# Performance work log

Measured on AMD Instinct MI355X. Metric: run time of the kernel, lower is better.

Reference implementation:

```python
import jax, jax.numpy as jnp
import numpy as np
import math

B, L, D = 2, 2048, 768
H, DK = 8, 64
DV = D // H  # 96
N_POS = 32
DFF = 2 * D
EPS = 1e-5


def setup_inputs() -> dict:
    key = jax.random.key(0)
    ks = jax.random.split(key, 12)
    s = 0.02
    return {
        "x": jax.random.normal(ks[0], (B, L, D), jnp.float32),
        "norm1_w": jnp.ones((D,), jnp.float32),
        "norm2_w": jnp.ones((D,), jnp.float32),
        "wq": jax.random.normal(ks[1], (D, H * DK), jnp.float32) * s,
        "wk": jax.random.normal(ks[2], (D, H * DK), jnp.float32) * s,
        "wv": jax.random.normal(ks[3], (D, H * DV), jnp.float32) * s,
        "wo": jax.random.normal(ks[4], (H * DV, D), jnp.float32) * s,
        "bo": jnp.zeros((D,), jnp.float32),
        "u_param": jax.random.normal(ks[5], (H, DK), jnp.float32) * s,
        "v_param": jax.random.normal(ks[6], (H, DK), jnp.float32) * s,
        "w_pos": jax.random.normal(ks[7], (H, DK, N_POS), jnp.float32) * s,
        "w1": jax.random.normal(ks[8], (D, DFF), jnp.float32) * s,
        "b1": jnp.zeros((DFF,), jnp.float32),
        "w2": jax.random.normal(ks[9], (DFF, D), jnp.float32) * s,
        "b2": jnp.zeros((D,), jnp.float32),
    }


def _rel_basis(l: int, n: int) -> jnp.ndarray:
    # Enformer-style central-mask relative position basis: [l, l, n]
    pos = jnp.arange(l)
    distance = pos[None, :] - pos[:, None]  # [l, l]
    pow_rate = jnp.exp(jnp.log(jnp.float32((l + 1) / 2.0)) / (n // 2))
    center_widths = pow_rate ** jnp.arange(1, n // 2 + 1, dtype=jnp.float32)
    d = distance[:, :, None].astype(jnp.float32)
    unsigned = (jnp.abs(d) <= center_widths).astype(jnp.float32)
    signed = jnp.sign(d) * unsigned
    return jnp.concatenate([unsigned, signed], axis=-1)  # [l, l, n]


def _rmsnorm(x, w):
    norm = jnp.mean(x * x, axis=-1, keepdims=True)
    return x * jax.lax.rsqrt(norm + EPS) * w


def reference(x, norm1_w, norm2_w, wq, wk, wv, wo, bo,
              u_param, v_param, w_pos, w1, b1, w2, b2):
    b, l, _ = x.shape
    skip = x
    h1 = _rmsnorm(x, norm1_w)

    q = (h1 @ wq).reshape(b, l, H, DK)
    k = (h1 @ wk).reshape(b, l, H, DK)
    v = (h1 @ wv).reshape(b, l, H, DV)

    basis = _rel_basis(l, N_POS)  # [l, l, n]
    scale = 1.0 / math.sqrt(DK)

    # qr_term: contract q with w_pos first, then with basis (avoids [h,l,l,d] r)
    qw = jnp.einsum('bihd,hdn->bihn', q, w_pos)          # [b,l,h,n]
    qr = jnp.einsum('bihn,ijn->bhij', qw, basis)          # [b,h,l,l]
    uk = jnp.einsum('hd,bjhd->bhj', u_param, k)[:, :, None, :]  # [b,h,1,l]
    vw = jnp.einsum('hd,hdn->hn', v_param, w_pos)         # [h,n]
    vr = jnp.einsum('hn,ijn->hij', vw, basis)[None]       # [1,h,l,l]

    bias = (qr + uk + vr) * scale
    scores = jnp.einsum('bihd,bjhd->bhij', q, k) * scale + bias
    attn = jax.nn.softmax(scores, axis=-1)
    out = jnp.einsum('bhij,bjhd->bihd', attn, v)          # [b,l,h,dv]

    out = out.reshape(b, l, H * DV) @ wo + bo
    x = out + skip

    skip = x
    h2 = _rmsnorm(x, norm2_w)
    h2 = jax.nn.gelu(h2 @ w1 + b1, approximate=False) @ w2 + b2
    return h2 + skip
```

## Files before the change

kernel.cpp:

```cpp
#include <hip/hip_runtime.h>

#define B_ 2
#define L_ 2048
#define D_ 768
#define H_ 8
#define DK_ 64
#define DV_ 96
#define NPOS_ 32

typedef __attribute__((ext_vector_type(8))) __bf16 bf16x8;
typedef __attribute__((ext_vector_type(4))) __bf16 bf16x4;
typedef __attribute__((ext_vector_type(4))) float f32x4;

static __device__ __forceinline__ float bs2f(short s) {
    return (float)__builtin_bit_cast(__bf16, s);
}
static __device__ __forceinline__ short f2bs(float f) {
    return __builtin_bit_cast(short, (__bf16)f);
}

__global__ __launch_bounds__(256) void prep_kernel(
    const float* __restrict__ wq, const float* __restrict__ wk,
    const float* __restrict__ wv, const float* __restrict__ wo,
    const float* __restrict__ w1, const float* __restrict__ w2,
    const float* __restrict__ vparam, const float* __restrict__ uparam,
    const float* __restrict__ wpos,
    short* __restrict__ wqkvT, short* __restrict__ woT,
    short* __restrict__ w1T, short* __restrict__ w2T,
    unsigned char* __restrict__ sidx, float* __restrict__ VU, float* __restrict__ VS,
    const float* __restrict__ x, const float* __restrict__ n1w, short* __restrict__ h1)
{
    __shared__ short T[64][66];
    __shared__ float vw[H_ * NPOS_];
    __shared__ float uw[H_ * NPOS_];
    __shared__ float red[4];
    int blk = blockIdx.x, tid = threadIdx.x;
    if (blk < 1056) {
        const float* W; short* Wt; int K, N, bx, by;
        if (blk < 96)       { W = wq; Wt = wqkvT;              K = 768;  N = 512;  int b = blk;       bx = b % 8;  by = b / 8; }
        else if (blk < 192) { W = wk; Wt = wqkvT + 512 * 768;  K = 768;  N = 512;  int b = blk - 96;  bx = b % 8;  by = b / 8; }
        else if (blk < 336) { W = wv; Wt = wqkvT + 1024 * 768; K = 768;  N = 768;  int b = blk - 192; bx = b % 12; by = b / 12; }
        else if (blk < 480) { W = wo; Wt = woT;                K = 768;  N = 768;  int b = blk - 336; bx = b % 12; by = b / 12; }
        else if (blk < 768) { W = w1; Wt = w1T;                K = 768;  N = 1536; int b = blk - 480; bx = b % 24; by = b / 24; }
        else                { W = w2; Wt = w2T;                K = 1536; N = 768;  int b = blk - 768; bx = b % 12; by = b / 12; }
        int n0 = bx << 6, k0 = by << 6;
        for (int idx = tid; idx < 4096; idx += 256) {
            int r = idx >> 6, c = idx & 63;
            T[c][r] = f2bs(W[(size_t)(k0 + r) * N + n0 + c]);
        }
        __syncthreads();
        for (int idx = tid; idx < 4096; idx += 256) {
            int r = idx >> 6, c = idx & 63;
            Wt[(size_t)(n0 + r) * K + k0 + c] = T[r][c];
        }
    } else if (blk == 1056) {
        float pr = expf(logf((L_ + 1) / 2.0f) / (NPOS_ / 2));
        for (int idx = tid; idx < 4095; idx += 256) {
            int d = idx - 2047;
            int ad = d < 0 ? -d : d;
            int c = 0;
            for (int m = 1; m <= NPOS_ / 2; ++m) {
                float cw = powf(pr, (float)m);
                if (cw < (float)ad) c++;
            }
            sidx[idx] = (unsigned char)(d > 0 ? c : (d < 0 ? 17 + c : 34));
        }
        {
            int h = tid >> 5, n = tid & 31;
            float av = 0.f, au = 0.f;
            for (int d = 0; d < DK_; ++d) {
                float wp = wpos[(h * DK_ + d) * NPOS_ + n];
                av += vparam[h * DK_ + d] * wp;
                au += uparam[h * DK_ + d] * wp;
            }
            vw[tid] = av;
            uw[tid] = au;
        }
        __syncthreads();
        if (tid < H_ * 17) {
            int h = tid / 17, m = tid % 17;
            float su = 0.f, ss = 0.f;
            for (int t2 = m; t2 < 16; ++t2) {
                su += vw[h * NPOS_ + t2] - uw[h * NPOS_ + t2];
                ss += vw[h * NPOS_ + 16 + t2] - uw[h * NPOS_ + 16 + t2];
            }
            VU[h * 17 + m] = su * 0.125f;
            VS[h * 17 + m] = ss * 0.125f;
        }
    } else {
        int row = blk - 1057;
        const float* xr = x + (size_t)row * D_;
        float ss = 0.f;
        for (int c = tid; c < D_; c += 256) { float f = xr[c]; ss += f * f; }
        for (int msk = 1; msk < 64; msk <<= 1) ss += __shfl_xor(ss, msk);
        if ((tid & 63) == 0) red[tid >> 6] = ss;
        __syncthreads();
        float tot = red[0] + red[1] + red[2] + red[3];
        float sc = rsqrtf(tot * (1.f / D_) + 1e-5f);
        for (int c = tid; c < D_; c += 256)
            h1[(size_t)row * D_ + c] = f2bs(xr[c] * sc * n1w[c]);
    }
}

__global__ __launch_bounds__(256) void rmsnorm_kernel(
    const float* __restrict__ x, const float* __restrict__ wgt, short* __restrict__ out)
{
    int row = blockIdx.x, tid = threadIdx.x;
    __shared__ float red[4];
    const float* xr = x + (size_t)row * D_;
    float ss = 0.f;
    for (int c = tid; c < D_; c += 256) { float f = xr[c]; ss += f * f; }
    for (int msk = 1; msk < 64; msk <<= 1) ss += __shfl_xor(ss, msk);
    if ((tid & 63) == 0) red[tid >> 6] = ss;
    __syncthreads();
    float tot = red[0] + red[1] + red[2] + red[3];
    float sc = rsqrtf(tot * (1.f / D_) + 1e-5f);
    for (int c = tid; c < D_; c += 256)
        out[(size_t)row * D_ + c] = f2bs(xr[c] * sc * wgt[c]);
}

__global__ __launch_bounds__(256) void gemm64(
    const short* __restrict__ A, const short* __restrict__ Bt,
    const float* __restrict__ bias, const float* __restrict__ resid,
    void* __restrict__ outp,
    int M, int N, int K, int act, int out_f32)
{
    __shared__ __align__(16) short Al[64 * 136];
    __shared__ __align__(16) short Bl[64 * 136];
    int tid = threadIdx.x;
    int w = tid >> 6, lane = tid & 63, quad = lane >> 4, t = lane & 15;
    int m0b = blockIdx.y << 6, n0b = blockIdx.x << 6;
    int wr = (w >> 1) << 5, wc = (w & 1) << 5;
    int rA = tid >> 4, c8 = (tid & 15) << 3;
    f32x4 acc[2][2] = {};
    bf16x8 pA[4], pB[4];
#pragma unroll
    for (int it = 0; it < 4; ++it) {
        pA[it] = *(const bf16x8*)&A[(size_t)(m0b + rA + (it << 4)) * K + c8];
        pB[it] = *(const bf16x8*)&Bt[(size_t)(n0b + rA + (it << 4)) * K + c8];
    }
    for (int kb = 0; kb < K; kb += 128) {
        __syncthreads();
#pragma unroll
        for (int it = 0; it < 4; ++it) {
            *(bf16x8*)&Al[(rA + (it << 4)) * 136 + c8] = pA[it];
            *(bf16x8*)&Bl[(rA + (it << 4)) * 136 + c8] = pB[it];
        }
        if (kb + 128 < K) {
#pragma unroll
            for (int it = 0; it < 4; ++it) {
                pA[it] = *(const bf16x8*)&A[(size_t)(m0b + rA + (it << 4)) * K + kb + 128 + c8];
                pB[it] = *(const bf16x8*)&Bt[(size_t)(n0b + rA + (it << 4)) * K + kb + 128 + c8];
            }
        }
        __syncthreads();
#pragma unroll
        for (int ks = 0; ks < 4; ++ks) {
            bf16x8 af0 = *(bf16x8*)&Al[(wr + t) * 136 + (ks << 5) + (quad << 3)];
            bf16x8 af1 = *(bf16x8*)&Al[(wr + 16 + t) * 136 + (ks << 5) + (quad << 3)];
            bf16x8 bf0 = *(bf16x8*)&Bl[(wc + t) * 136 + (ks << 5) + (quad << 3)];
            bf16x8 bf1 = *(bf16x8*)&Bl[(wc + 16 + t) * 136 + (ks << 5) + (quad << 3)];
            acc[0][0] = __builtin_amdgcn_mfma_f32_16x16x32_bf16(af0, bf0, acc[0][0], 0, 0, 0);
            acc[0][1] = __builtin_amdgcn_mfma_f32_16x16x32_bf16(af0, bf1, acc[0][1], 0, 0, 0);
            acc[1][0] = __builtin_amdgcn_mfma_f32_16x16x32_bf16(af1, bf0, acc[1][0], 0, 0, 0);
            acc[1][1] = __builtin_amdgcn_mfma_f32_16x16x32_bf16(af1, bf1, acc[1][1], 0, 0, 0);
        }
    }
#pragma unroll
    for (int ms = 0; ms < 2; ++ms)
#pragma unroll
        for (int ns = 0; ns < 2; ++ns)
#pragma unroll
            for (int r = 0; r < 4; ++r) {
                int row = m0b + wr + (ms << 4) + (quad << 2) + r;
                int col = n0b + wc + (ns << 4) + t;
                float v2 = acc[ms][ns][r];
                if (bias) v2 += bias[col];
                if (act == 1) v2 = 0.5f * v2 * (1.f + erff(v2 * 0.70710678118654752f));
                if (resid) v2 += resid[(size_t)row * N + col];
                if (out_f32) ((float*)outp)[(size_t)row * N + col] = v2;
                else ((short*)outp)[(size_t)row * N + col] = f2bs(v2);
            }
}

__global__ __launch_bounds__(256) void gemm128(
    const short* __restrict__ A, const short* __restrict__ Bt,
    const float* __restrict__ bias, const float* __restrict__ uadd,
    void* __restrict__ outp, int M, int N, int K, int act)
{
    __shared__ __align__(16) short Al[128 * 72];
    __shared__ __align__(16) short Bl[128 * 72];
    int tid = threadIdx.x;
    int w = tid >> 6, lane = tid & 63, quad = lane >> 4, t = lane & 15;
    int m0b = blockIdx.y << 7, n0b = blockIdx.x << 7;
    int wm = (w >> 1) << 6, wn = (w & 1) << 6;
    int r0 = tid >> 3, c8 = (tid & 7) << 3;
    f32x4 acc[4][4] = {};
    bf16x8 pA[4], pB[4];
#pragma unroll
    for (int it = 0; it < 4; ++it) {
        pA[it] = *(const bf16x8*)&A[(size_t)(m0b + r0 + (it << 5)) * K + c8];
        pB[it] = *(const bf16x8*)&Bt[(size_t)(n0b + r0 + (it << 5)) * K + c8];
    }
    for (int kb = 0; kb < K; kb += 64) {
        __syncthreads();
#pragma unroll
        for (int it = 0; it < 4; ++it) {
            *(bf16x8*)&Al[(r0 + (it << 5)) * 72 + c8] = pA[it];
            *(bf16x8*)&Bl[(r0 + (it << 5)) * 72 + c8] = pB[it];
        }
        if (kb + 64 < K) {
#pragma unroll
            for (int it = 0; it < 4; ++it) {
                pA[it] = *(const bf16x8*)&A[(size_t)(m0b + r0 + (it << 5)) * K + kb + 64 + c8];
                pB[it] = *(const bf16x8*)&Bt[(size_t)(n0b + r0 + (it << 5)) * K + kb + 64 + c8];
            }
        }
        __syncthreads();
#pragma unroll
        for (int ks = 0; ks < 2; ++ks) {
            bf16x8 af[4], bf[4];
#pragma unroll
            for (int ms = 0; ms < 4; ++ms)
                af[ms] = *(bf16x8*)&Al[(wm + ms * 16 + t) * 72 + (ks << 5) + (quad << 3)];
#pragma unroll
            for (int ns = 0; ns < 4; ++ns)
                bf[ns] = *(bf16x8*)&Bl[(wn + ns * 16 + t) * 72 + (ks << 5) + (quad << 3)];
#pragma unroll
            for (int ms = 0; ms < 4; ++ms)
#pragma unroll
                for (int ns = 0; ns < 4; ++ns)
                    acc[ms][ns] = __builtin_amdgcn_mfma_f32_16x16x32_bf16(af[ms], bf[ns], acc[ms][ns], 0, 0, 0);
        }
    }
#pragma unroll
    for (int ms = 0; ms < 4; ++ms)
#pragma unroll
        for (int ns = 0; ns < 4; ++ns)
#pragma unroll
            for (int r = 0; r < 4; ++r) {
                int row = m0b + wm + ms * 16 + (quad << 2) + r;
                int col = n0b + wn + ns * 16 + t;
                float v2 = acc[ms][ns][r];
                if (uadd && col < 512) v2 = 0.125f * (v2 + uadd[col]);
                if (bias) v2 += bias[col];
                if (act == 1) v2 = 0.5f * v2 * (1.f + erff(v2 * 0.70710678118654752f));
                ((short*)outp)[(size_t)row * N + col] = f2bs(v2);
            }
}

__global__ __launch_bounds__(256) void qv_kernel(
    const short* __restrict__ qkv, const float* __restrict__ wpos,
    const float* __restrict__ VU, const float* __restrict__ VS,
    float* __restrict__ Tg, short* __restrict__ vT, short* __restrict__ kT)
{
    __shared__ __align__(16) char arena[69696];
    int blk = blockIdx.x, tid = threadIdx.x;
    if (blk < 256) {
        float* wl   = (float*)arena;
        float* qrow = (float*)(arena + 65536);
        float* qw   = (float*)(arena + 67584);
        float* sU   = (float*)(arena + 68608);
        float* sS   = (float*)(arena + 69152);
        for (int idx = tid; idx < 4096; idx += 256)
            ((float4*)wl)[idx] = ((const float4*)wpos)[idx];
        int r0 = blk << 4;
        int h = tid >> 5, n = tid & 31;
        for (int rr = 0; rr < 16; ++rr) {
            int row = r0 + rr;
            __syncthreads();
            const short* base = qkv + (size_t)row * 1792;
            qrow[tid]       = bs2f(base[tid]);
            qrow[tid + 256] = bs2f(base[tid + 256]);
            __syncthreads();
            float acc = 0.f;
            for (int d = 0; d < DK_; ++d)
                acc += qrow[h * DK_ + d] * wl[(h * DK_ + d) * 32 + n];
            qw[tid] = acc;
            __syncthreads();
            if (tid < 136) {
                int hh = tid / 17, m = tid % 17;
                float su = 0.f, ss = 0.f;
                for (int t2 = m; t2 < 16; ++t2) { su += qw[hh * NPOS_ + t2]; ss += qw[hh * NPOS_ + 16 + t2]; }
                sU[tid] = su + VU[tid];
                sS[tid] = ss + VS[tid];
            }
            __syncthreads();
            if (tid < 280) {
                int h2 = tid / 35, s = tid % 35;
                int m = s < 17 ? s : (s < 34 ? s - 17 : 0);
                float su = sU[h2 * 17 + m], ss = sS[h2 * 17 + m];
                Tg[(size_t)row * 280 + tid] = s < 17 ? su + ss : (s < 34 ? su - ss : su);
            }
        }
    } else if (blk < 512) {
        short* T = (short*)arena;
        int vb = blk - 256;
        int bh = vb >> 4, b = bh >> 3, h = bh & 7;
        int j0 = (vb & 15) << 7;
#pragma unroll
        for (int it = 0; it < 6; ++it) {
            int idx = tid + (it << 8);
            int row = idx / 12, c8 = (idx % 12) << 3;
            *(bf16x8*)&T[row * 104 + c8] =
                *(const bf16x8*)&qkv[(size_t)(b * L_ + j0 + row) * 1792 + 1024 + h * DV_ + c8];
        }
        __syncthreads();
#pragma unroll
        for (int it = 0; it < 6; ++it) {
            int idx = tid + (it << 8);
            int sub = idx / 768;
            int rem = idx - sub * 768;
            int f = rem >> 6, l = rem & 63;
            int dv = f >> 1, ks = f & 1;
            int q = l >> 4, t = l & 15;
            bf16x8 o;
#pragma unroll
            for (int e = 0; e < 8; ++e) {
                int jl = ((e & 3) << 4) + (ks << 3) + (q << 1) + (e >> 2);
                o[e] = __builtin_bit_cast(__bf16, T[(sub * 64 + jl) * 104 + dv * 16 + t]);
            }
            int jt = ((vb & 15) << 1) + sub;
            *(bf16x8*)&vT[((((size_t)bh * 32 + jt) * 12 + f) * 64 + l) * 8] = o;
        }
    } else {
        short* T = (short*)arena;
        int vb = blk - 512;
        int bh = vb >> 4, b = bh >> 3, h = bh & 7;
        int c128 = vb & 15;
        int j0 = c128 << 7;
#pragma unroll
        for (int it = 0; it < 4; ++it) {
            int idx = tid + (it << 8);
            int row = idx >> 3, c8 = (idx & 7) << 3;
            *(bf16x8*)&T[row * 72 + c8] =
                *(const bf16x8*)&qkv[(size_t)(b * L_ + j0 + row) * 1792 + 512 + h * DK_ + c8];
        }
        __syncthreads();
#pragma unroll
        for (int it = 0; it < 4; ++it) {
            int idx = tid + (it << 8);
            int sub = idx >> 9;
            int rem = idx & 511;
            int f = rem >> 6, l = rem & 63;
            int q = l >> 4, tt = l & 15;
            bf16x8 o = *(bf16x8*)&T[(sub * 64 + (f >> 1) * 16 + tt) * 72 + ((f & 1) << 5) + (q << 3)];
            int jt = (c128 << 1) + sub;
            *(bf16x8*)&kT[((((size_t)bh * 32 + jt) * 8 + f) * 64 + l) * 8] = o;
        }
    }
}

__global__ __launch_bounds__(256, 4) void flash_kernel(
    const short* __restrict__ qkv, const short* __restrict__ kT,
    const short* __restrict__ vT, const float* __restrict__ Tg,
    const unsigned char* __restrict__ sidx_g, short* __restrict__ ao)
{
    __shared__ __align__(16) char arena[17920];
    int tid = threadIdx.x;
    int w = tid >> 6, lane = tid & 63, quad = lane >> 4, t = lane & 15;
    int iw = w >> 1, jg = w & 1;
    short* Pl = (short*)(arena + w * 2304);
    float* Tt = (float*)(arena + 9216);
    unsigned char* sidxl = (unsigned char*)(arena + 13824);

    int id = blockIdx.x;
    int bh8 = id & 7, rest = id >> 3;
    int x = rest & 63, hi = rest >> 6;
    int bh = bh8 + (hi << 3);
    int b = bh >> 3, h = bh & 7;
    int i0 = x << 5;

    for (int idx = tid; idx < 32 * 35; idx += 256) {
        int il = idx / 35, s = idx - il * 35;
        Tt[il * 36 + s] = Tg[(size_t)(b * L_ + i0 + il) * 280 + h * 35 + s];
    }
    for (int idx = tid; idx < 4095; idx += 256) sidxl[idx] = sidx_g[idx];
    __syncthreads();

    int iq = i0 + iw * 16 + t;
    const short* qbase = qkv + (size_t)(b * L_ + iq) * 1792 + h * DK_;
    bf16x8 qf0 = *(const bf16x8*)(qbase + (quad << 3));
    bf16x8 qf1 = *(const bf16x8*)(qbase + 32 + (quad << 3));

    f32x4 O[6] = {};
    float lsum[4] = {0.f, 0.f, 0.f, 0.f};
    const short* kfb = kT + (size_t)bh * 32 * 8 * 512 + lane * 8;
    const short* vfb = vT + (size_t)bh * 32 * 12 * 512 + lane * 8;

    for (int tix = 0; tix < 16; ++tix) {
        int jt = (tix << 1) + jg;
        int j0 = jt << 6;
        bf16x8 kf[8];
#pragma unroll
        for (int f = 0; f < 8; ++f)
            kf[f] = *(const bf16x8*)(kfb + ((size_t)jt * 8 + f) * 512);
        __builtin_amdgcn_sched_barrier(0);

        f32x4 S[4];
        __builtin_amdgcn_s_setprio(1);
#pragma unroll
        for (int ct = 0; ct < 4; ++ct) {
            f32x4 z = {};
            z = __builtin_amdgcn_mfma_f32_16x16x32_bf16(qf0, kf[ct * 2], z, 0, 0, 0);
            S[ct] = __builtin_amdgcn_mfma_f32_16x16x32_bf16(qf1, kf[ct * 2 + 1], z, 0, 0, 0);
        }
        __builtin_amdgcn_s_setprio(0);

        bf16x8 vf[12];
#pragma unroll
        for (int f = 0; f < 12; ++f)
            vf[f] = *(const bf16x8*)(vfb + ((size_t)jt * 12 + f) * 512);
        __builtin_amdgcn_sched_barrier(0);

#pragma unroll
        for (int r = 0; r < 4; ++r) {
            int il = (quad << 2) + r;
            int i = i0 + iw * 16 + il;
            const float* Trow = &Tt[(iw * 16 + il) * 36];
            bf16x4 pv;
#pragma unroll
            for (int ct = 0; ct < 4; ++ct) {
                int j = j0 + ct * 16 + t;
                int s = sidxl[j - i + 2047];
                float p = __expf(S[ct][r] + Trow[s]);
                __bf16 pb = (__bf16)p;
                pv[ct] = pb;
                lsum[r] += (float)pb;
            }
            *(bf16x4*)&Pl[il * 72 + t * 4] = pv;
        }
        __builtin_amdgcn_s_setprio(1);
#pragma unroll
        for (int ks = 0; ks < 2; ++ks) {
            bf16x8 pa = *(bf16x8*)&Pl[t * 72 + (ks << 5) + (quad << 3)];
#pragma unroll
            for (int dv = 0; dv < 6; ++dv)
                O[dv] = __builtin_amdgcn_mfma_f32_16x16x32_bf16(pa, vf[dv * 2 + ks], O[dv], 0, 0, 0);
        }
        __builtin_amdgcn_s_setprio(0);
    }

    __syncthreads();
    float* F = (float*)arena;
    int fl = (iw << 6) + lane;
    if (jg == 1) {
#pragma unroll
        for (int dv = 0; dv < 6; ++dv)
#pragma unroll
            for (int r = 0; r < 4; ++r)
                F[((dv << 2) + r) * 128 + fl] = O[dv][r];
#pragma unroll
        for (int r = 0; r < 4; ++r) F[(24 + r) * 128 + fl] = lsum[r];
    }
    __syncthreads();
    if (jg == 0) {
#pragma unroll
        for (int r = 0; r < 4; ++r) {
            float lr = lsum[r] + F[(24 + r) * 128 + fl];
            lr += __shfl_xor(lr, 1);
            lr += __shfl_xor(lr, 2);
            lr += __shfl_xor(lr, 4);
            lr += __shfl_xor(lr, 8);
            float inv = 1.f / lr;
            int i = i0 + iw * 16 + (quad << 2) + r;
            size_t base = (size_t)(b * L_ + i) * D_ + h * DV_;
#pragma unroll
            for (int dv = 0; dv < 6; ++dv)
                ao[base + dv * 16 + t] = f2bs((O[dv][r] + F[((dv << 2) + r) * 128 + fl]) * inv);
        }
    }
}

extern "C" void kernel_launch(void* const* d_in, const int* in_sizes, int n_in,
                              void* d_out, int out_size, void* d_ws, size_t ws_size,
                              hipStream_t stream)
{
    const float* x    = (const float*)d_in[0];
    const float* n1w  = (const float*)d_in[1];
    const float* n2w  = (const float*)d_in[2];
    const float* wq   = (const float*)d_in[3];
    const float* wk   = (const float*)d_in[4];
    const float* wv   = (const float*)d_in[5];
    const float* wo   = (const float*)d_in[6];
    const float* bo   = (const float*)d_in[7];
    const float* up   = (const float*)d_in[8];
    const float* vp   = (const float*)d_in[9];
    const float* wpos = (const float*)d_in[10];
    const float* w1   = (const float*)d_in[11];
    const float* b1   = (const float*)d_in[12];
    const float* w2   = (const float*)d_in[13];
    const float* b2   = (const float*)d_in[14];

    char* ws = (char*)d_ws;
    short* h1   = (short*)(ws + 0);
    short* qkv  = (short*)(ws + 6291456);
    float* Tg   = (float*)(ws + 20971520);
    float* VUg  = (float*)(ws + 25559040);
    float* VSg  = (float*)(ws + 25560064);
    unsigned char* sidx = (unsigned char*)(ws + 25561088);
    short* ao   = (short*)(ws + 25569280);
    float* x2   = (float*)(ws + 31860736);
    short* vT   = (short*)(ws + 31860736);
    short* kT   = (short*)(ws + 38152192);
    short* wqkvT= (short*)(ws + 44443648);
    short* woT  = (short*)(ws + 47196160);
    short* w1T  = (short*)(ws + 48375808);
    short* w2T  = (short*)(ws + 50735104);
    short* f1   = (short*)(ws + 0);
    short* h2n  = (short*)(ws + 14680064);

    prep_kernel<<<5153, 256, 0, stream>>>(wq, wk, wv, wo, w1, w2, vp, up, wpos,
                                          wqkvT, woT, w1T, w2T, sidx, VUg, VSg,
                                          x, n1w, h1);
    gemm128<<<dim3(14, 32), 256, 0, stream>>>(h1, wqkvT, nullptr, up, qkv, 4096, 1792, 768, 0);
    qv_kernel<<<768, 256, 0, stream>>>(qkv, wpos, VUg, VSg, Tg, vT, kT);
    flash_kernel<<<dim3(1024), 256, 0, stream>>>(qkv, kT, vT, Tg, sidx, ao);
    gemm64<<<dim3(12, 64), 256, 0, stream>>>(ao, woT, bo, x, x2, 4096, 768, 768, 0, 1);
    rmsnorm_kernel<<<4096, 256, 0, stream>>>(x2, n2w, h2n);
    gemm128<<<dim3(12, 32), 256, 0, stream>>>(h2n, w1T, b1, nullptr, f1, 4096, 1536, 768, 1);
    gemm64<<<dim3(12, 64), 256, 0, stream>>>(f1, w2T, b2, x2, d_out, 4096, 768, 1536, 0, 1);
}
```

Measured before the change: 307.9 us.

## Unify GEMMs into templated kernel with direct global-to-LDS loads and swizzle

Replaces the two GEMM kernels with one templated 512-thread kernel. It loads tiles straight from global memory into LDS with global_load_lds, double-buffers LDS, and uses an XOR swizzle in place of padding. The aim is to skip the register staging of tiles, cut the syncs per k-step to one, and avoid bank conflicts. The 64-wide variant now uses 128-row tiles, which halves its block count and may reduce occupancy or parallelism on the N=768 GEMMs.

```diff
diff --git a/kernel.cpp b/kernel.cpp
--- a/kernel.cpp
+++ b/kernel.cpp
@@ -17,6 +17,12 @@
 }
 static __device__ __forceinline__ short f2bs(float f) {
     return __builtin_bit_cast(short, (__bf16)f);
+}
+
+typedef __attribute__((address_space(1))) void gas_void;
+typedef __attribute__((address_space(3))) void las_void;
+static __device__ __forceinline__ void gload16(const short* g, char* l) {
+    __builtin_amdgcn_global_load_lds((const gas_void*)g, (las_void*)l, 16, 0, 0);
 }
 
 __global__ __launch_bounds__(256) void prep_kernel(
@@ -119,124 +125,71 @@
         out[(size_t)row * D_ + c] = f2bs(xr[c] * sc * wgt[c]);
 }
 
-__global__ __launch_bounds__(256) void gemm64(
+template<int BN>
+__global__ __launch_bounds__(512, 4) void gemmx(
     const short* __restrict__ A, const short* __restrict__ Bt,
-    const float* __restrict__ bias, const float* __restrict__ resid,
-    void* __restrict__ outp,
+    const float* __restrict__ bias, const float* __restrict__ uadd,
+    const float* __restrict__ resid, void* __restrict__ outp,
     int M, int N, int K, int act, int out_f32)
 {
-    __shared__ __align__(16) short Al[64 * 136];
-    __shared__ __align__(16) short Bl[64 * 136];
+    constexpr int STRIDE = 16384 + BN * 128;
+    __shared__ __align__(16) char ldsb[2 * STRIDE];
     int tid = threadIdx.x;
     int w = tid >> 6, lane = tid & 63, quad = lane >> 4, t = lane & 15;
-    int m0b = blockIdx.y << 6, n0b = blockIdx.x << 6;
-    int wr = (w >> 1) << 5, wc = (w & 1) << 5;
-    int rA = tid >> 4, c8 = (tid & 15) << 3;
-    f32x4 acc[2][2] = {};
-    bf16x8 pA[4], pB[4];
-#pragma unroll
-    for (int it = 0; it < 4; ++it) {
-        pA[it] = *(const bf16x8*)&A[(size_t)(m0b + rA + (it << 4)) * K + c8];
-        pB[it] = *(const bf16x8*)&Bt[(size_t)(n0b + rA + (it << 4)) * K + c8];
-    }
-    for (int kb = 0; kb < K; kb += 128) {
-        __syncthreads();
-#pragma unroll
-        for (int it = 0; it < 4; ++it) {
-            *(bf16x8*)&Al[(rA + (it << 4)) * 136 + c8] = pA[it];
-            *(bf16x8*)&Bl[(rA + (it << 4)) * 136 + c8] = pB[it];
-        }
-        if (kb + 128 < K) {
-#pragma unroll
-            for (int it = 0; it < 4; ++it) {
-                pA[it] = *(const bf16x8*)&A[(size_t)(m0b + rA + (it << 4)) * K + kb + 128 + c8];
-                pB[it] = *(const bf16x8*)&Bt[(size_t)(n0b + rA + (it << 4)) * K + kb + 128 + c8];
-            }
-        }
-        __syncthreads();
-#pragma unroll
-        for (int ks = 0; ks < 4; ++ks) {
-            bf16x8 af0 = *(bf16x8*)&Al[(wr + t) * 136 + (ks << 5) + (quad << 3)];
-            bf16x8 af1 = *(bf16x8*)&Al[(wr + 16 + t) * 136 + (ks << 5) + (quad << 3)];
-            bf16x8 bf0 = *(bf16x8*)&Bl[(wc + t) * 136 + (ks << 5) + (quad << 3)];
-            bf16x8 bf1 = *(bf16x8*)&Bl[(wc + 16 + t) * 136 + (ks << 5) + (quad << 3)];
-            acc[0][0] = __builtin_amdgcn_mfma_f32_16x16x32_bf16(af0, bf0, acc[0][0], 0, 0, 0);
-            acc[0][1] = __builtin_amdgcn_mfma_f32_16x16x32_bf16(af0, bf1, acc[0][1], 0, 0, 0);
-            acc[1][0] = __builtin_amdgcn_mfma_f32_16x16x32_bf16(af1, bf0, acc[1][0], 0, 0, 0);
-            acc[1][1] = __builtin_amdgcn_mfma_f32_16x16x32_bf16(af1, bf1, acc[1][1], 0, 0, 0);
-        }
+    int wm = (w >> 1) << 5;
+    int wn = (w & 1) * (BN / 2);
+    int m0b = blockIdx.y << 7, n0b = blockIdx.x * BN;
+
+    int srow = tid >> 3;
+    int scol = ((tid & 7) ^ (srow & 7)) << 3;
+    const short* aSrc0 = A + (size_t)(m0b + srow) * K + scol;
+    const short* aSrc1 = A + (size_t)(m0b + 64 + srow) * K + scol;
+    const short* bSrc0 = Bt + (size_t)(n0b + srow) * K + scol;
+    const short* bSrc1 = Bt + (size_t)(n0b + 64 + srow) * K + scol;
+    int wo1024 = w << 10;
+
+    f32x4 acc[2][BN / 32] = {};
+
+    gload16(aSrc0, ldsb + wo1024);
+    gload16(aSrc1, ldsb + 8192 + wo1024);
+    gload16(bSrc0, ldsb + 16384 + wo1024);
+    if (BN == 128) gload16(bSrc1, ldsb + 16384 + 8192 + wo1024);
+
+    int swz = (t & 7) << 4;
+    int cur = 0;
+    for (int kb = 0; kb < K; kb += 64) {
+        __syncthreads();
+        if (kb + 64 < K) {
+            char* nb = ldsb + (cur ^ 1) * STRIDE;
+            gload16(aSrc0 + kb + 64, nb + wo1024);
+            gload16(aSrc1 + kb + 64, nb + 8192 + wo1024);
+            gload16(bSrc0 + kb + 64, nb + 16384 + wo1024);
+            if (BN == 128) gload16(bSrc1 + kb + 64, nb + 16384 + 8192 + wo1024);
+        }
+        char* Ab = ldsb + cur * STRIDE;
+        char* Bb = Ab + 16384;
+#pragma unroll
+        for (int ks = 0; ks < 2; ++ks) {
+            int cb = ((ks << 6) + (quad << 4)) ^ swz;
+            bf16x8 af[2], bf[BN / 32];
+#pragma unroll
+            for (int ms = 0; ms < 2; ++ms)
+                af[ms] = *(const bf16x8*)(Ab + (wm + ms * 16 + t) * 128 + cb);
+#pragma unroll
+            for (int ns = 0; ns < BN / 32; ++ns)
+                bf[ns] = *(const bf16x8*)(Bb + (wn + ns * 16 + t) * 128 + cb);
+#pragma unroll
+            for (int ms = 0; ms < 2; ++ms)
+#pragma unroll
+                for (int ns = 0; ns < BN / 32; ++ns)
+                    acc[ms][ns] = __builtin_amdgcn_mfma_f32_16x16x32_bf16(af[ms], bf[ns], acc[ms][ns], 0, 0, 0);
+        }
+        cur ^= 1;
     }
 #pragma unroll
     for (int ms = 0; ms < 2; ++ms)
 #pragma unroll
-        for (int ns = 0; ns < 2; ++ns)
-#pragma unroll
-            for (int r = 0; r < 4; ++r) {
-                int row = m0b + wr + (ms << 4) + (quad << 2) + r;
-                int col = n0b + wc + (ns << 4) + t;
-                float v2 = acc[ms][ns][r];
-                if (bias) v2 += bias[col];
-                if (act == 1) v2 = 0.5f * v2 * (1.f + erff(v2 * 0.70710678118654752f));
-                if (resid) v2 += resid[(size_t)row * N + col];
-                if (out_f32) ((float*)outp)[(size_t)row * N + col] = v2;
-                else ((short*)outp)[(size_t)row * N + col] = f2bs(v2);
-            }
-}
-
-__global__ __launch_bounds__(256) void gemm128(
-    const short* __restrict__ A, const short* __restrict__ Bt,
-    const float* __restrict__ bias, const float* __restrict__ uadd,
-    void* __restrict__ outp, int M, int N, int K, int act)
-{
-    __shared__ __align__(16) short Al[128 * 72];
-    __shared__ __align__(16) short Bl[128 * 72];
-    int tid = threadIdx.x;
-    int w = tid >> 6, lane = tid & 63, quad = lane >> 4, t = lane & 15;
-    int m0b = blockIdx.y << 7, n0b = blockIdx.x << 7;
-    int wm = (w >> 1) << 6, wn = (w & 1) << 6;
-    int r0 = tid >> 3, c8 = (tid & 7) << 3;
-    f32x4 acc[4][4] = {};
-    bf16x8 pA[4], pB[4];
-#pragma unroll
-    for (int it = 0; it < 4; ++it) {
-        pA[it] = *(const bf16x8*)&A[(size_t)(m0b + r0 + (it << 5)) * K + c8];
-        pB[it] = *(const bf16x8*)&Bt[(size_t)(n0b + r0 + (it << 5)) * K + c8];
-    }
-    for (int kb = 0; kb < K; kb += 64) {
-        __syncthreads();
-#pragma unroll
-        for (int it = 0; it < 4; ++it) {
-            *(bf16x8*)&Al[(r0 + (it << 5)) * 72 + c8] = pA[it];
-            *(bf16x8*)&Bl[(r0 + (it << 5)) * 72 + c8] = pB[it];
-        }
-        if (kb + 64 < K) {
-#pragma unroll
-            for (int it = 0; it < 4; ++it) {
-                pA[it] = *(const bf16x8*)&A[(size_t)(m0b + r0 + (it << 5)) * K + kb + 64 + c8];
-                pB[it] = *(const bf16x8*)&Bt[(size_t)(n0b + r0 + (it << 5)) * K + kb + 64 + c8];
-            }
-        }
-        __syncthreads();
-#pragma unroll
-        for (int ks = 0; ks < 2; ++ks) {
-            bf16x8 af[4], bf[4];
-#pragma unroll
-            for (int ms = 0; ms < 4; ++ms)
-                af[ms] = *(bf16x8*)&Al[(wm + ms * 16 + t) * 72 + (ks << 5) + (quad << 3)];
-#pragma unroll
-            for (int ns = 0; ns < 4; ++ns)
-                bf[ns] = *(bf16x8*)&Bl[(wn + ns * 16 + t) * 72 + (ks << 5) + (quad << 3)];
-#pragma unroll
-            for (int ms = 0; ms < 4; ++ms)
-#pragma unroll
-                for (int ns = 0; ns < 4; ++ns)
-                    acc[ms][ns] = __builtin_amdgcn_mfma_f32_16x16x32_bf16(af[ms], bf[ns], acc[ms][ns], 0, 0, 0);
-        }
-    }
-#pragma unroll
-    for (int ms = 0; ms < 4; ++ms)
-#pragma unroll
-        for (int ns = 0; ns < 4; ++ns)
+        for (int ns = 0; ns < BN / 32; ++ns)
 #pragma unroll
             for (int r = 0; r < 4; ++r) {
                 int row = m0b + wm + ms * 16 + (quad << 2) + r;
@@ -245,7 +198,9 @@
                 if (uadd && col < 512) v2 = 0.125f * (v2 + uadd[col]);
                 if (bias) v2 += bias[col];
                 if (act == 1) v2 = 0.5f * v2 * (1.f + erff(v2 * 0.70710678118654752f));
-                ((short*)outp)[(size_t)row * N + col] = f2bs(v2);
+                if (resid) v2 += resid[(size_t)row * N + col];
+                if (out_f32) ((float*)outp)[(size_t)row * N + col] = v2;
+                else ((short*)outp)[(size_t)row * N + col] = f2bs(v2);
             }
 }
 
@@ -513,11 +468,11 @@
     prep_kernel<<<5153, 256, 0, stream>>>(wq, wk, wv, wo, w1, w2, vp, up, wpos,
                                           wqkvT, woT, w1T, w2T, sidx, VUg, VSg,
                                           x, n1w, h1);
-    gemm128<<<dim3(14, 32), 256, 0, stream>>>(h1, wqkvT, nullptr, up, qkv, 4096, 1792, 768, 0);
+    gemmx<128><<<dim3(14, 32), 512, 0, stream>>>(h1, wqkvT, nullptr, up, nullptr, qkv, 4096, 1792, 768, 0, 0);
     qv_kernel<<<768, 256, 0, stream>>>(qkv, wpos, VUg, VSg, Tg, vT, kT);
     flash_kernel<<<dim3(1024), 256, 0, stream>>>(qkv, kT, vT, Tg, sidx, ao);
-    gemm64<<<dim3(12, 64), 256, 0, stream>>>(ao, woT, bo, x, x2, 4096, 768, 768, 0, 1);
+    gemmx<64><<<dim3(12, 32), 512, 0, stream>>>(ao, woT, bo, nullptr, x, x2, 4096, 768, 768, 0, 1);
     rmsnorm_kernel<<<4096, 256, 0, stream>>>(x2, n2w, h2n);
-    gemm128<<<dim3(12, 32), 256, 0, stream>>>(h2n, w1T, b1, nullptr, f1, 4096, 1536, 768, 1);
-    gemm64<<<dim3(12, 64), 256, 0, stream>>>(f1, w2T, b2, x2, d_out, 4096, 768, 1536, 0, 1);
-}
+    gemmx<128><<<dim3(12, 32), 512, 0, stream>>>(h2n, w1T, b1, nullptr, nullptr, f1, 4096, 1536, 768, 1, 0);
+    gemmx<64><<<dim3(12, 32), 512, 0, stream>>>(f1, w2T, b2, nullptr, x2, d_out, 4096, 768, 1536, 0, 1);
+}
```

New measurement: 286.3 us. -7.0%, faster.
